# Optimization experiments

Measured on AMD Instinct MI355X. Metric: run time of the kernel, lower is better.

Reference implementation:

```python
import jax, jax.numpy as jnp
import numpy as np

N_HEAD = 16
N_EMBD = 2048
HEAD_DIM = N_EMBD // N_HEAD  # 128
B, T = 4, 2048
BASE_THETA = 10000.0


def _rotary_tables(seq_len, dim, dtype):
    inv_freq = 1.0 / (BASE_THETA ** (jnp.arange(0, dim, 2, dtype=jnp.float32) / dim))
    t = jnp.arange(seq_len, dtype=jnp.float32)
    freqs = jnp.outer(t, inv_freq)  # [T, dim/2]
    cos = jnp.cos(freqs)[None, :, None, :].astype(dtype)
    sin = jnp.sin(freqs)[None, :, None, :].astype(dtype)
    return cos, sin


def _apply_rotary(x, cos, sin):
    # x: [B, T, H, D]; rotate pairs (x[..., :D/2], x[..., D/2:])
    d = x.shape[3] // 2
    x1, x2 = x[..., :d], x[..., d:]
    y1 = x1 * cos + x2 * sin
    y2 = -x1 * sin + x2 * cos
    return jnp.concatenate([y1, y2], axis=3).astype(x.dtype)


def setup_inputs() -> dict:
    key = jax.random.key(0)
    ks = jax.random.split(key, 5)
    scale = 1.0 / np.sqrt(N_EMBD)
    return {
        "x": jax.random.normal(ks[0], (B, T, N_EMBD), dtype=jnp.float32),
        "wq": jax.random.normal(ks[1], (N_EMBD, N_EMBD), dtype=jnp.float32) * scale,
        "wk": jax.random.normal(ks[2], (N_EMBD, N_EMBD), dtype=jnp.float32) * scale,
        "wv": jax.random.normal(ks[3], (N_EMBD, N_EMBD), dtype=jnp.float32) * scale,
        "wo": jax.random.normal(ks[4], (N_EMBD, N_EMBD), dtype=jnp.float32) * scale,
    }


def reference(x, wq, wk, wv, wo):
    Bc, Tc, C = x.shape
    H, D = N_HEAD, HEAD_DIM
    # bias-free projections (nn.Linear applies x @ W.T)
    q = (x @ wq.T).reshape(Bc, Tc, H, D)
    k = (x @ wk.T).reshape(Bc, Tc, H, D)
    v = (x @ wv.T).reshape(Bc, Tc, H, D)
    cos, sin = _rotary_tables(Tc, D, x.dtype)
    # original module applies rotary TWICE (once before a dead SDPA, once after)
    q = _apply_rotary(_apply_rotary(q, cos, sin), cos, sin)
    k = _apply_rotary(_apply_rotary(k, cos, sin), cos, sin)
    # causal attention (flex_attention with causal block_mask, default scale)
    scores = jnp.einsum("bthd,bshd->bhts", q, k) / jnp.sqrt(jnp.asarray(D, x.dtype))
    causal = jnp.tril(jnp.ones((Tc, Tc), dtype=bool))
    scores = jnp.where(causal[None, None, :, :], scores, jnp.asarray(-jnp.inf, scores.dtype))
    attn = jax.nn.softmax(scores, axis=-1)
    y = jnp.einsum("bhts,bshd->bthd", attn, v).reshape(Bc, Tc, C)
    return y @ wo.T
```

## Files before the change

### kernel.cpp

```cpp
#include <hip/hip_runtime.h>
#include <math.h>

typedef unsigned short u16;
typedef __attribute__((ext_vector_type(4))) float f32x4;
typedef __attribute__((ext_vector_type(8))) __bf16 bf16x8;
typedef __attribute__((ext_vector_type(4))) unsigned short u16x4;
typedef __attribute__((ext_vector_type(8))) unsigned short u16x8;

#define GLL16(gp, lp) __builtin_amdgcn_global_load_lds( \
    (__attribute__((address_space(1))) void*)(void*)(gp), \
    (__attribute__((address_space(3))) void*)(void*)(lp), 16, 0, 0)

__device__ __forceinline__ u16 f2bf(float x) {
    unsigned u = __float_as_uint(x);
    return (u16)((u + 0x7FFFu + ((u >> 16) & 1u)) >> 16);
}
__device__ __forceinline__ float bf2f(u16 h) { return __uint_as_float(((unsigned)h) << 16); }

__device__ __forceinline__ f32x4 mfma16(bf16x8 a, bf16x8 b, f32x4 c) {
    return __builtin_amdgcn_mfma_f32_16x16x32_bf16(a, b, c, 0, 0, 0);
}

__global__ void cvt_f32_bf16(const float* __restrict__ s, u16* __restrict__ d, int n4) {
    int i = blockIdx.x * 256 + threadIdx.x;
    if (i < n4) {
        float4 v = ((const float4*)s)[i];
        u16x4 o = { f2bf(v.x), f2bf(v.y), f2bf(v.z), f2bf(v.w) };
        ((u16x4*)d)[i] = o;
    }
}

__global__ void rope_table_k(float2* __restrict__ tab) {
    int id = blockIdx.x * 256 + threadIdx.x;
    int t = id >> 6, j = id & 63;
    float freq = exp2f(-((float)(2 * j) / 128.f) * 13.287712379549449f);
    float ang = 2.f * (float)t * freq;
    float sv, cv;
    sincosf(ang, &sv, &cv);
    float2 r; r.x = cv; r.y = sv;
    tab[id] = r;
}

template <int MODE>
__global__ __launch_bounds__(256) void gemm_nt(const u16* __restrict__ A, const u16* __restrict__ Bw,
                                               u16* __restrict__ Qo, u16* __restrict__ Ko,
                                               u16* __restrict__ Vt, float* __restrict__ Out,
                                               const float2* __restrict__ tab, float qscale, int K) {
    __shared__ u16 smem[32768];
    const int tid = threadIdx.x;
    const int lane = tid & 63;
    const int qd = lane >> 4, ln = lane & 15;
    const int wid = tid >> 6;
    const int wx = wid & 1, wy = wid >> 1;

    constexpr int NBY = (MODE == 0) ? 48 : 16;
    const int id = blockIdx.y * 64 + blockIdx.x;
    const int xcd = id & 7, slot = id >> 3;
    const int m0 = ((slot / NBY) * 8 + xcd) * 128;
    const int n0 = (slot % NBY) * 128;

    int asrc[4], bsrc[4], ldst[4];
#pragma unroll
    for (int l = 0; l < 4; ++l) {
        const int i = l * 256 + tid;
        const int r = i >> 3;
        const int kc = (i & 7) ^ (r & 7);
        asrc[l] = (m0 + r) * K + kc * 8;
        bsrc[l] = (n0 + r) * K + kc * 8;
        ldst[l] = i * 8;
    }
    const u16* Ag = A;
    const u16* Bg = Bw;

    f32x4 acc[4][4];
#pragma unroll
    for (int mi = 0; mi < 4; ++mi)
#pragma unroll
        for (int ni = 0; ni < 4; ++ni) acc[mi][ni] = f32x4{0.f, 0.f, 0.f, 0.f};

    const int arow = (wy * 64 + ln) * 64;
    const int brow = (wx * 64 + ln) * 64;
    const int cx[2] = { (qd ^ (ln & 7)) * 8, ((qd + 4) ^ (ln & 7)) * 8 };

    auto compute = [&](int buf) {
        const u16* As = &smem[buf * 16384];
        const u16* Bs = As + 8192;
#pragma unroll
        for (int ks = 0; ks < 2; ++ks) {
            bf16x8 af[4], bfr[4];
#pragma unroll
            for (int i = 0; i < 4; ++i) af[i] = *(const bf16x8*)&As[arow + i * 1024 + cx[ks]];
#pragma unroll
            for (int i = 0; i < 4; ++i) bfr[i] = *(const bf16x8*)&Bs[brow + i * 1024 + cx[ks]];
#pragma unroll
            for (int mi = 0; mi < 4; ++mi)
#pragma unroll
                for (int ni = 0; ni < 4; ++ni)
                    acc[mi][ni] = mfma16(af[mi], bfr[ni], acc[mi][ni]);
        }
    };

    const int niter = K >> 6;
#pragma unroll
    for (int l = 0; l < 4; ++l) GLL16(Ag + asrc[l], &smem[ldst[l]]);
#pragma unroll
    for (int l = 0; l < 4; ++l) GLL16(Bg + bsrc[l], &smem[8192 + ldst[l]]);
    Ag += 64; Bg += 64;

    for (int kt = 0; kt < niter - 1; ++kt) {
        asm volatile("s_barrier" ::: "memory");
        u16* dA = &smem[((kt + 1) & 1) * 16384];
#pragma unroll
        for (int l = 0; l < 4; ++l) GLL16(Ag + asrc[l], &dA[ldst[l]]);
#pragma unroll
        for (int l = 0; l < 4; ++l) GLL16(Bg + bsrc[l], &dA[8192 + ldst[l]]);
        Ag += 64; Bg += 64;
        asm volatile("s_waitcnt vmcnt(8)" ::: "memory");
        asm volatile("s_barrier" ::: "memory");
        compute(kt & 1);
    }
    asm volatile("s_barrier" ::: "memory");
    asm volatile("s_waitcnt vmcnt(0)" ::: "memory");
    asm volatile("s_barrier" ::: "memory");
    compute((niter - 1) & 1);

    __syncthreads();

    if constexpr (MODE == 0) {
        const int sec = n0 >> 11;
        if (sec <= 1) {
#pragma unroll
            for (int mi = 0; mi < 4; ++mi)
#pragma unroll
                for (int ni = 0; ni < 4; ++ni) {
                    const int col = wx * 64 + ni * 16 + ln;
                    const int cc = col >> 3, co = col & 7;
#pragma unroll
                    for (int r = 0; r < 4; ++r) {
                        const int row = wy * 64 + mi * 16 + qd * 4 + r;
                        smem[row * 128 + ((cc ^ (row & 15)) * 8) + co] = f2bf(acc[mi][ni][r]);
                    }
                }
            __syncthreads();
            const float qs = (sec == 0) ? qscale : 1.0f;
            u16* dstb = (sec == 0 ? Qo : Ko);
#pragma unroll
            for (int it = 0; it < 4; ++it) {
                const int c = it * 256 + tid;
                const int m = c >> 3, d8 = c & 7;
                const u16x8 lo = *(const u16x8*)&smem[m * 128 + ((d8 ^ (m & 15)) * 8)];
                const u16x8 hi = *(const u16x8*)&smem[m * 128 + (((d8 + 8) ^ (m & 15)) * 8)];
                const int t = (m0 + m) & 2047;
                const float2* tb = tab + t * 64 + d8 * 8;
                u16x8 o1, o2;
#pragma unroll
                for (int i = 0; i < 8; ++i) {
                    const float x1 = bf2f(lo[i]), x2 = bf2f(hi[i]);
                    const float2 cs = tb[i];
                    o1[i] = f2bf((x1 * cs.x + x2 * cs.y) * qs);
                    o2[i] = f2bf((x2 * cs.x - x1 * cs.y) * qs);
                }
                u16* dst = dstb + (size_t)(m0 + m) * 2048 + (n0 & 2047) + d8 * 8;
                *(u16x8*)dst = o1;
                *(u16x8*)(dst + 64) = o2;
            }
        } else {
            const int bb = m0 >> 11;
#pragma unroll
            for (int mi = 0; mi < 4; ++mi) {
                const int mbase = wy * 64 + mi * 16 + qd * 4;
                const int mch = mbase >> 3, moff = mbase & 7;
#pragma unroll
                for (int ni = 0; ni < 4; ++ni) {
                    const int nl = wx * 64 + ni * 16 + ln;
                    u16x4 pk = { f2bf(acc[mi][ni][0]), f2bf(acc[mi][ni][1]),
                                 f2bf(acc[mi][ni][2]), f2bf(acc[mi][ni][3]) };
                    *(u16x4*)&smem[nl * 128 + ((mch ^ (nl & 15)) * 8) + moff] = pk;
                }
            }
            __syncthreads();
#pragma unroll
            for (int i = 0; i < 8; ++i) {
                const int c = i * 256 + tid;
                const int nl = c >> 4;
                const u16x8 v = *(const u16x8*)&smem[c * 8];
                const int mch = (c & 15) ^ (nl & 15);
                const int hd = (n0 - 4096) + nl;
                *(u16x8*)&Vt[((size_t)(bb * 2048 + hd)) * 2048 + (m0 & 2047) + mch * 8] = v;
            }
        }
    } else {
        const int mg0 = m0 + wy * 64 + qd * 4;
        const int ng0 = n0 + wx * 64 + ln;
#pragma unroll
        for (int mi = 0; mi < 4; ++mi)
#pragma unroll
            for (int ni = 0; ni < 4; ++ni) {
                const int ng = ng0 + ni * 16;
#pragma unroll
                for (int r = 0; r < 4; ++r)
                    Out[(size_t)(mg0 + mi * 16 + r) * 2048 + ng] = acc[mi][ni][r];
            }
    }
}

__global__ __launch_bounds__(512, 4) void attn_kernel(const u16* __restrict__ Qb, const u16* __restrict__ Kb,
                                                      const u16* __restrict__ Vt, u16* __restrict__ Yb) {
    extern __shared__ u16 smem[];
    u16* QP = smem;
    u16* KsB = smem + 8192;
    u16* VsB = smem + 8192 + 16384;

    const int tid = threadIdx.x;
    const int lane = tid & 63;
    const int qd = lane >> 4, ln = lane & 15;
    const int wid = tid >> 6;
    const int id = (int)blockIdx.x;
    const int px = id >> 6;
    const int bh = id & 63;
    const int b = bh >> 4, h = bh & 15;

    const u16* Qbh = Qb + ((size_t)b * 2048 * 16 + h) * 128;
    const u16* Kbh = Kb + ((size_t)b * 2048 * 16 + h) * 128;
    const u16* Vbh = Vt + ((size_t)(b * 16 + h) * 128) * 2048;

    int lC[2], kOff[2], vOff[2];
#pragma unroll
    for (int p = 0; p < 2; ++p) {
        const int c = p * 512 + tid;
        lC[p] = c * 8;
        { const int r = c >> 4, cc = (c & 15) ^ (r & 7); kOff[p] = r * 2048 + cc * 8; }
        { const int rv = c >> 3, cc = (c & 7) ^ (rv & 7); vOff[p] = rv * 2048 + cc * 8; }
    }

    bf16x8 onesf;
#pragma unroll
    for (int i = 0; i < 8; ++i) onesf[i] = (__bf16)1.0f;

    for (int half = 0; half < 2; ++half) {
        const int qt = half ? px : (15 - px);
        const int q0 = qt * 128;
        const int wq = q0 + wid * 16;
        const int nkt = 2 * qt + 2;

        __syncthreads();
#pragma unroll
        for (int p = 0; p < 2; ++p)
            GLL16(Qbh + (size_t)q0 * 2048 + kOff[p], &QP[lC[p]]);
        __syncthreads();
        bf16x8 qf[4];
        if (wid < 4) {
            const int lr = wid * 16 + ln;
#pragma unroll
            for (int ks = 0; ks < 4; ++ks)
                qf[ks] = *(const bf16x8*)&QP[lr * 128 + (((ks * 4 + qd) ^ (lr & 7)) * 8)];
        }
        __syncthreads();
#pragma unroll
        for (int p = 0; p < 2; ++p)
            GLL16(Qbh + (size_t)(q0 + 64) * 2048 + kOff[p], &QP[lC[p]]);
        __syncthreads();
        if (wid >= 4) {
            const int lr = (wid - 4) * 16 + ln;
#pragma unroll
            for (int ks = 0; ks < 4; ++ks)
                qf[ks] = *(const bf16x8*)&QP[lr * 128 + (((ks * 4 + qd) ^ (lr & 7)) * 8)];
        }
        __syncthreads();

#pragma unroll
        for (int p = 0; p < 2; ++p) GLL16(Kbh + kOff[p], &KsB[lC[p]]);
#pragma unroll
        for (int p = 0; p < 2; ++p) GLL16(Vbh + vOff[p], &VsB[lC[p]]);

        f32x4 o[8];
#pragma unroll
        for (int di = 0; di < 8; ++di) o[di] = f32x4{0.f, 0.f, 0.f, 0.f};
        f32x4 lacc = f32x4{0.f, 0.f, 0.f, 0.f};
        float Mr[4];
#pragma unroll
        for (int r = 0; r < 4; ++r) Mr[r] = -1e30f;

        for (int kt = 0; kt < nkt; ++kt) {
            const int k0 = kt * 64;
            asm volatile("s_barrier" ::: "memory");
            if (kt + 1 < nkt) {
                u16* kd = KsB + ((kt + 1) & 1) * 8192;
                u16* vd = VsB + ((kt + 1) & 1) * 8192;
#pragma unroll
                for (int p = 0; p < 2; ++p) GLL16(Kbh + (size_t)(k0 + 64) * 2048 + kOff[p], &kd[lC[p]]);
#pragma unroll
                for (int p = 0; p < 2; ++p) GLL16(Vbh + (size_t)(k0 + 64) + vOff[p], &vd[lC[p]]);
                asm volatile("s_waitcnt vmcnt(4)" ::: "memory");
            } else {
                asm volatile("s_waitcnt vmcnt(0)" ::: "memory");
            }
            asm volatile("s_barrier" ::: "memory");

            if (k0 <= wq + 15) {
                const u16* Kc = KsB + (kt & 1) * 8192;
                const u16* Vc = VsB + (kt & 1) * 8192;
                f32x4 s[4];
#pragma unroll
                for (int ni = 0; ni < 4; ++ni) s[ni] = f32x4{0.f, 0.f, 0.f, 0.f};
#pragma unroll
                for (int ks = 0; ks < 4; ++ks) {
                    bf16x8 kf[4];
#pragma unroll
                    for (int ni = 0; ni < 4; ++ni) {
                        const int row = ni * 16 + ln;
                        kf[ni] = *(const bf16x8*)&Kc[row * 128 + (((ks * 4 + qd) ^ (ln & 7)) * 8)];
                    }
#pragma unroll
                    for (int ni = 0; ni < 4; ++ni)
                        s[ni] = mfma16(qf[ks], kf[ni], s[ni]);
                }
                if (k0 + 63 > wq) {
#pragma unroll
                    for (int ni = 0; ni < 4; ++ni)
#pragma unroll
                        for (int r = 0; r < 4; ++r) {
                            const int qi = wq + qd * 4 + r;
                            const int ki = k0 + ni * 16 + ln;
                            if (ki > qi) s[ni][r] = -1e30f;
                        }
                }
                float rx[4];
#pragma unroll
                for (int r = 0; r < 4; ++r)
                    rx[r] = fmaxf(fmaxf(s[0][r], s[1][r]), fmaxf(s[2][r], s[3][r]));
#pragma unroll
                for (int st = 1; st < 16; st <<= 1)
#pragma unroll
                    for (int r = 0; r < 4; ++r)
                        rx[r] = fmaxf(rx[r], __shfl_xor(rx[r], st));
                float al[4];
                bool need = false;
#pragma unroll
                for (int r = 0; r < 4; ++r) {
                    const float nm = fmaxf(Mr[r], rx[r]);
                    al[r] = exp2f(Mr[r] - nm);
                    Mr[r] = nm;
                    need |= (al[r] != 1.0f);
                }
                if (__any(need)) {
#pragma unroll
                    for (int r = 0; r < 4; ++r) lacc[r] *= al[r];
#pragma unroll
                    for (int di = 0; di < 8; ++di)
#pragma unroll
                        for (int r = 0; r < 4; ++r) o[di][r] *= al[r];
                }
#pragma unroll
                for (int ni = 0; ni < 4; ++ni) {
                    const int cc0 = ni * 2 + (ln >> 3);
#pragma unroll
                    for (int r = 0; r < 4; ++r) {
                        const float p = exp2f(s[ni][r] - Mr[r]);
                        const int prow = wid * 16 + qd * 4 + r;
                        QP[prow * 64 + ((cc0 ^ ((prow >> 1) & 7)) * 8) + (ln & 7)] = f2bf(p);
                    }
                }
#pragma unroll
                for (int ks2 = 0; ks2 < 2; ++ks2) {
                    const int prow = wid * 16 + ln;
                    bf16x8 pf = *(const bf16x8*)&QP[prow * 64 + (((ks2 * 4 + qd) ^ ((prow >> 1) & 7)) * 8)];
                    lacc = mfma16(pf, onesf, lacc);
#pragma unroll
                    for (int di = 0; di < 8; ++di) {
                        const int row = di * 16 + ln;
                        bf16x8 vf = *(const bf16x8*)&Vc[row * 64 + (((ks2 * 4 + qd) ^ (ln & 7)) * 8)];
                        o[di] = mfma16(pf, vf, o[di]);
                    }
                }
            }
        }

        float inv[4];
#pragma unroll
        for (int r = 0; r < 4; ++r) inv[r] = 1.f / lacc[r];
#pragma unroll
        for (int di = 0; di < 8; ++di)
#pragma unroll
            for (int r = 0; r < 4; ++r) {
                const int t = q0 + wid * 16 + qd * 4 + r;
                const int d = di * 16 + ln;
                Yb[((size_t)((b * 2048 + t) * 16 + h)) * 128 + d] = f2bf(o[di][r] * inv[r]);
            }
    }
}

extern "C" void kernel_launch(void* const* d_in, const int* in_sizes, int n_in,
                              void* d_out, int out_size, void* d_ws, size_t ws_size,
                              hipStream_t stream) {
    const float* x  = (const float*)d_in[0];
    const float* wq = (const float*)d_in[1];
    const float* wk = (const float*)d_in[2];
    const float* wv = (const float*)d_in[3];
    const float* wo = (const float*)d_in[4];
    float* out = (float*)d_out;
    char* ws = (char*)d_ws;

    u16* xb     = (u16*)(ws);
    u16* wqkv   = (u16*)(ws + (size_t)33554432);
    u16* wob    = (u16*)(ws + (size_t)58720256);
    u16* Qb     = (u16*)(ws + (size_t)67108864);
    u16* Kb     = (u16*)(ws + (size_t)100663296);
    u16* Vt     = (u16*)(ws + (size_t)134217728);
    float2* tab = (float2*)(ws + (size_t)167772160);
    u16* Yb = xb;

    const float scl = 0.08838834764831845f * 1.4426950408889634f;

    cvt_f32_bf16<<<16384, 256, 0, stream>>>(x, xb, 4194304);
    cvt_f32_bf16<<<4096, 256, 0, stream>>>(wq, wqkv, 1048576);
    cvt_f32_bf16<<<4096, 256, 0, stream>>>(wk, wqkv + 4194304, 1048576);
    cvt_f32_bf16<<<4096, 256, 0, stream>>>(wv, wqkv + 8388608, 1048576);
    cvt_f32_bf16<<<4096, 256, 0, stream>>>(wo, wob, 1048576);
    rope_table_k<<<512, 256, 0, stream>>>(tab);

    gemm_nt<0><<<dim3(64, 48), 256, 0, stream>>>(xb, wqkv, Qb, Kb, Vt, nullptr, tab, scl, 2048);

    hipFuncSetAttribute((const void*)attn_kernel, hipFuncAttributeMaxDynamicSharedMemorySize, 81920);
    attn_kernel<<<dim3(512), 512, 81920, stream>>>(Qb, Kb, Vt, Yb);

    gemm_nt<1><<<dim3(64, 16), 256, 0, stream>>>(Yb, wob, nullptr, nullptr, nullptr, out, tab, 1.0f, 2048);
}
```

Measured before the change: 641.3 us.

## Enlarge GEMM tiles to 256x256 with 8 waves and quarter-staged prefetch pipeline

Both projection GEMMs now use 256x256 output tiles computed by 512-thread blocks, each wave owning a 128x64 sub-tile, with 128KB of dynamic LDS for double buffering. The K loop is split into four MFMA phases. Each phase issues the prefetch of one quarter of the next tile and raises wave priority around the MFMA bursts. The aim is more data reuse per LDS load and better overlap of global loads with compute. In exchange, the grid has fewer blocks (768 and 256), so the output GEMM may not fill all CUs, and register pressure is higher.

```diff
diff --git a/kernel.cpp b/kernel.cpp
--- a/kernel.cpp
+++ b/kernel.cpp
@@ -42,114 +42,157 @@
 }
 
 template <int MODE>
-__global__ __launch_bounds__(256) void gemm_nt(const u16* __restrict__ A, const u16* __restrict__ Bw,
-                                               u16* __restrict__ Qo, u16* __restrict__ Ko,
-                                               u16* __restrict__ Vt, float* __restrict__ Out,
-                                               const float2* __restrict__ tab, float qscale, int K) {
-    __shared__ u16 smem[32768];
+__global__ __launch_bounds__(512, 2) void gemm_nt(const u16* __restrict__ A, const u16* __restrict__ Bw,
+                                                  u16* __restrict__ Qo, u16* __restrict__ Ko,
+                                                  u16* __restrict__ Vt, float* __restrict__ Out,
+                                                  const float2* __restrict__ tab, float qscale, int K) {
+    extern __shared__ u16 smem[];
     const int tid = threadIdx.x;
     const int lane = tid & 63;
     const int qd = lane >> 4, ln = lane & 15;
     const int wid = tid >> 6;
-    const int wx = wid & 1, wy = wid >> 1;
-
-    constexpr int NBY = (MODE == 0) ? 48 : 16;
-    const int id = blockIdx.y * 64 + blockIdx.x;
+    const int wr = wid >> 2, wc = wid & 3;
+
+    constexpr int NBY = (MODE == 0) ? 24 : 8;
+    const int id = (int)blockIdx.x;
     const int xcd = id & 7, slot = id >> 3;
-    const int m0 = ((slot / NBY) * 8 + xcd) * 128;
-    const int n0 = (slot % NBY) * 128;
-
-    int asrc[4], bsrc[4], ldst[4];
-#pragma unroll
-    for (int l = 0; l < 4; ++l) {
-        const int i = l * 256 + tid;
-        const int r = i >> 3;
-        const int kc = (i & 7) ^ (r & 7);
-        asrc[l] = (m0 + r) * K + kc * 8;
-        bsrc[l] = (n0 + r) * K + kc * 8;
-        ldst[l] = i * 8;
-    }
-    const u16* Ag = A;
-    const u16* Bg = Bw;
-
-    f32x4 acc[4][4];
-#pragma unroll
-    for (int mi = 0; mi < 4; ++mi)
+    const int m0 = ((slot / NBY) * 8 + xcd) * 256;
+    const int n0 = (slot % NBY) * 256;
+
+    int sr[2], skc[2];
+#pragma unroll
+    for (int l = 0; l < 2; ++l) {
+        const int i = l * 512 + tid;
+        sr[l] = i >> 3;
+        skc[l] = (i & 7) ^ (sr[l] & 7);
+    }
+
+    auto stage = [&](int tt, int hx) {
+        const u16* gp = (hx < 2) ? A : Bw;
+        const int x0 = (hx < 2) ? m0 : n0;
+        const int h = hx & 1;
+        u16* lb = &smem[(tt & 1) * 32768 + (hx >> 1) * 16384 + h * 8192];
+#pragma unroll
+        for (int l = 0; l < 2; ++l)
+            GLL16(gp + (size_t)(x0 + 128 * h + sr[l]) * K + tt * 64 + skc[l] * 8,
+                  &lb[(l * 512 + tid) * 8]);
+    };
+
+    f32x4 acc[8][4];
+#pragma unroll
+    for (int mi = 0; mi < 8; ++mi)
 #pragma unroll
         for (int ni = 0; ni < 4; ++ni) acc[mi][ni] = f32x4{0.f, 0.f, 0.f, 0.f};
 
-    const int arow = (wy * 64 + ln) * 64;
-    const int brow = (wx * 64 + ln) * 64;
-    const int cx[2] = { (qd ^ (ln & 7)) * 8, ((qd + 4) ^ (ln & 7)) * 8 };
-
-    auto compute = [&](int buf) {
-        const u16* As = &smem[buf * 16384];
-        const u16* Bs = As + 8192;
-#pragma unroll
-        for (int ks = 0; ks < 2; ++ks) {
-            bf16x8 af[4], bfr[4];
-#pragma unroll
-            for (int i = 0; i < 4; ++i) af[i] = *(const bf16x8*)&As[arow + i * 1024 + cx[ks]];
-#pragma unroll
-            for (int i = 0; i < 4; ++i) bfr[i] = *(const bf16x8*)&Bs[brow + i * 1024 + cx[ks]];
-#pragma unroll
-            for (int mi = 0; mi < 4; ++mi)
-#pragma unroll
-                for (int ni = 0; ni < 4; ++ni)
-                    acc[mi][ni] = mfma16(af[mi], bfr[ni], acc[mi][ni]);
-        }
-    };
+    const int arow = (wr * 128 + ln) * 64;
+    const int brow = (wc * 64 + ln) * 64;
+    const int cxk[2] = { (qd ^ (ln & 7)) * 8, ((qd + 4) ^ (ln & 7)) * 8 };
 
     const int niter = K >> 6;
-#pragma unroll
-    for (int l = 0; l < 4; ++l) GLL16(Ag + asrc[l], &smem[ldst[l]]);
-#pragma unroll
-    for (int l = 0; l < 4; ++l) GLL16(Bg + bsrc[l], &smem[8192 + ldst[l]]);
-    Ag += 64; Bg += 64;
-
-    for (int kt = 0; kt < niter - 1; ++kt) {
+    stage(0, 0); stage(0, 1); stage(0, 2); stage(0, 3);
+    stage(1, 0);
+
+#pragma unroll 2
+    for (int t = 0; t < niter; ++t) {
+        const u16* As = &smem[(t & 1) * 32768];
+        const u16* Bs = As + 16384;
+        const bool pf = (t + 1 < niter);
+        if (pf) asm volatile("s_waitcnt vmcnt(2)" ::: "memory");
+        else    asm volatile("s_waitcnt vmcnt(0)" ::: "memory");
         asm volatile("s_barrier" ::: "memory");
-        u16* dA = &smem[((kt + 1) & 1) * 16384];
-#pragma unroll
-        for (int l = 0; l < 4; ++l) GLL16(Ag + asrc[l], &dA[ldst[l]]);
-#pragma unroll
-        for (int l = 0; l < 4; ++l) GLL16(Bg + bsrc[l], &dA[8192 + ldst[l]]);
-        Ag += 64; Bg += 64;
-        asm volatile("s_waitcnt vmcnt(8)" ::: "memory");
+        bf16x8 a0[4][2], b0[2][2];
+#pragma unroll
+        for (int mi = 0; mi < 4; ++mi)
+#pragma unroll
+            for (int ks = 0; ks < 2; ++ks)
+                a0[mi][ks] = *(const bf16x8*)&As[arow + mi * 1024 + cxk[ks]];
+#pragma unroll
+        for (int ni = 0; ni < 2; ++ni)
+#pragma unroll
+            for (int ks = 0; ks < 2; ++ks)
+                b0[ni][ks] = *(const bf16x8*)&Bs[brow + ni * 1024 + cxk[ks]];
+        if (pf) stage(t + 1, 1);
+        __builtin_amdgcn_s_setprio(1);
+#pragma unroll
+        for (int mi = 0; mi < 4; ++mi)
+#pragma unroll
+            for (int ni = 0; ni < 2; ++ni)
+#pragma unroll
+                for (int ks = 0; ks < 2; ++ks)
+                    acc[mi][ni] = mfma16(a0[mi][ks], b0[ni][ks], acc[mi][ni]);
+        __builtin_amdgcn_s_setprio(0);
         asm volatile("s_barrier" ::: "memory");
-        compute(kt & 1);
-    }
-    asm volatile("s_barrier" ::: "memory");
-    asm volatile("s_waitcnt vmcnt(0)" ::: "memory");
-    asm volatile("s_barrier" ::: "memory");
-    compute((niter - 1) & 1);
-
+        bf16x8 b1[2][2];
+#pragma unroll
+        for (int ni = 0; ni < 2; ++ni)
+#pragma unroll
+            for (int ks = 0; ks < 2; ++ks)
+                b1[ni][ks] = *(const bf16x8*)&Bs[brow + (ni + 2) * 1024 + cxk[ks]];
+        if (pf) stage(t + 1, 2);
+        __builtin_amdgcn_s_setprio(1);
+#pragma unroll
+        for (int mi = 0; mi < 4; ++mi)
+#pragma unroll
+            for (int ni = 0; ni < 2; ++ni)
+#pragma unroll
+                for (int ks = 0; ks < 2; ++ks)
+                    acc[mi][ni + 2] = mfma16(a0[mi][ks], b1[ni][ks], acc[mi][ni + 2]);
+        __builtin_amdgcn_s_setprio(0);
+        asm volatile("s_barrier" ::: "memory");
+        bf16x8 a1[4][2];
+#pragma unroll
+        for (int mi = 0; mi < 4; ++mi)
+#pragma unroll
+            for (int ks = 0; ks < 2; ++ks)
+                a1[mi][ks] = *(const bf16x8*)&As[arow + (mi + 4) * 1024 + cxk[ks]];
+        if (pf) stage(t + 1, 3);
+        __builtin_amdgcn_s_setprio(1);
+#pragma unroll
+        for (int mi = 0; mi < 4; ++mi)
+#pragma unroll
+            for (int ni = 0; ni < 2; ++ni)
+#pragma unroll
+                for (int ks = 0; ks < 2; ++ks)
+                    acc[mi + 4][ni] = mfma16(a1[mi][ks], b0[ni][ks], acc[mi + 4][ni]);
+        __builtin_amdgcn_s_setprio(0);
+        asm volatile("s_barrier" ::: "memory");
+        if (t + 2 < niter) stage(t + 2, 0);
+        __builtin_amdgcn_s_setprio(1);
+#pragma unroll
+        for (int mi = 0; mi < 4; ++mi)
+#pragma unroll
+            for (int ni = 0; ni < 2; ++ni)
+#pragma unroll
+                for (int ks = 0; ks < 2; ++ks)
+                    acc[mi + 4][ni + 2] = mfma16(a1[mi][ks], b1[ni][ks], acc[mi + 4][ni + 2]);
+        __builtin_amdgcn_s_setprio(0);
+    }
     __syncthreads();
 
     if constexpr (MODE == 0) {
         const int sec = n0 >> 11;
         if (sec <= 1) {
 #pragma unroll
-            for (int mi = 0; mi < 4; ++mi)
+            for (int mi = 0; mi < 8; ++mi)
 #pragma unroll
                 for (int ni = 0; ni < 4; ++ni) {
-                    const int col = wx * 64 + ni * 16 + ln;
+                    const int col = wc * 64 + ni * 16 + ln;
                     const int cc = col >> 3, co = col & 7;
 #pragma unroll
                     for (int r = 0; r < 4; ++r) {
-                        const int row = wy * 64 + mi * 16 + qd * 4 + r;
-                        smem[row * 128 + ((cc ^ (row & 15)) * 8) + co] = f2bf(acc[mi][ni][r]);
+                        const int row = wr * 128 + mi * 16 + qd * 4 + r;
+                        smem[row * 256 + ((cc ^ (row & 15)) * 8) + co] = f2bf(acc[mi][ni][r]);
                     }
                 }
             __syncthreads();
             const float qs = (sec == 0) ? qscale : 1.0f;
             u16* dstb = (sec == 0 ? Qo : Ko);
 #pragma unroll
-            for (int it = 0; it < 4; ++it) {
-                const int c = it * 256 + tid;
-                const int m = c >> 3, d8 = c & 7;
-                const u16x8 lo = *(const u16x8*)&smem[m * 128 + ((d8 ^ (m & 15)) * 8)];
-                const u16x8 hi = *(const u16x8*)&smem[m * 128 + (((d8 + 8) ^ (m & 15)) * 8)];
+            for (int it = 0; it < 8; ++it) {
+                const int c = it * 512 + tid;
+                const int m = c >> 4, hh = (c >> 3) & 1, d8 = c & 7;
+                const u16x8 lo = *(const u16x8*)&smem[m * 256 + (((hh * 16 + d8) ^ (m & 15)) * 8)];
+                const u16x8 hi = *(const u16x8*)&smem[m * 256 + (((hh * 16 + 8 + d8) ^ (m & 15)) * 8)];
                 const int t = (m0 + m) & 2047;
                 const float2* tb = tab + t * 64 + d8 * 8;
                 u16x8 o1, o2;
@@ -160,40 +203,40 @@
                     o1[i] = f2bf((x1 * cs.x + x2 * cs.y) * qs);
                     o2[i] = f2bf((x2 * cs.x - x1 * cs.y) * qs);
                 }
-                u16* dst = dstb + (size_t)(m0 + m) * 2048 + (n0 & 2047) + d8 * 8;
+                u16* dst = dstb + (size_t)(m0 + m) * 2048 + (n0 & 2047) + hh * 128 + d8 * 8;
                 *(u16x8*)dst = o1;
                 *(u16x8*)(dst + 64) = o2;
             }
         } else {
             const int bb = m0 >> 11;
 #pragma unroll
-            for (int mi = 0; mi < 4; ++mi) {
-                const int mbase = wy * 64 + mi * 16 + qd * 4;
+            for (int mi = 0; mi < 8; ++mi) {
+                const int mbase = wr * 128 + mi * 16 + qd * 4;
                 const int mch = mbase >> 3, moff = mbase & 7;
 #pragma unroll
                 for (int ni = 0; ni < 4; ++ni) {
-                    const int nl = wx * 64 + ni * 16 + ln;
+                    const int nl = wc * 64 + ni * 16 + ln;
                     u16x4 pk = { f2bf(acc[mi][ni][0]), f2bf(acc[mi][ni][1]),
                                  f2bf(acc[mi][ni][2]), f2bf(acc[mi][ni][3]) };
-                    *(u16x4*)&smem[nl * 128 + ((mch ^ (nl & 15)) * 8) + moff] = pk;
+                    *(u16x4*)&smem[nl * 256 + ((mch ^ (nl & 15)) * 8) + moff] = pk;
                 }
             }
             __syncthreads();
 #pragma unroll
-            for (int i = 0; i < 8; ++i) {
-                const int c = i * 256 + tid;
-                const int nl = c >> 4;
-                const u16x8 v = *(const u16x8*)&smem[c * 8];
-                const int mch = (c & 15) ^ (nl & 15);
+            for (int i = 0; i < 16; ++i) {
+                const int c = i * 512 + tid;
+                const int nl = c >> 5, ch = c & 31;
+                const u16x8 v = *(const u16x8*)&smem[nl * 256 + ch * 8];
+                const int mch = ch ^ (nl & 15);
                 const int hd = (n0 - 4096) + nl;
                 *(u16x8*)&Vt[((size_t)(bb * 2048 + hd)) * 2048 + (m0 & 2047) + mch * 8] = v;
             }
         }
     } else {
-        const int mg0 = m0 + wy * 64 + qd * 4;
-        const int ng0 = n0 + wx * 64 + ln;
-#pragma unroll
-        for (int mi = 0; mi < 4; ++mi)
+        const int mg0 = m0 + wr * 128 + qd * 4;
+        const int ng0 = n0 + wc * 64 + ln;
+#pragma unroll
+        for (int mi = 0; mi < 8; ++mi)
 #pragma unroll
             for (int ni = 0; ni < 4; ++ni) {
                 const int ng = ng0 + ni * 16;
@@ -419,10 +462,13 @@
     cvt_f32_bf16<<<4096, 256, 0, stream>>>(wo, wob, 1048576);
     rope_table_k<<<512, 256, 0, stream>>>(tab);
 
-    gemm_nt<0><<<dim3(64, 48), 256, 0, stream>>>(xb, wqkv, Qb, Kb, Vt, nullptr, tab, scl, 2048);
+    hipFuncSetAttribute((const void*)gemm_nt<0>, hipFuncAttributeMaxDynamicSharedMemorySize, 131072);
+    hipFuncSetAttribute((const void*)gemm_nt<1>, hipFuncAttributeMaxDynamicSharedMemorySize, 131072);
+
+    gemm_nt<0><<<dim3(768), 512, 131072, stream>>>(xb, wqkv, Qb, Kb, Vt, nullptr, tab, scl, 2048);
 
     hipFuncSetAttribute((const void*)attn_kernel, hipFuncAttributeMaxDynamicSharedMemorySize, 81920);
     attn_kernel<<<dim3(512), 512, 81920, stream>>>(Qb, Kb, Vt, Yb);
 
-    gemm_nt<1><<<dim3(64, 16), 256, 0, stream>>>(Yb, wob, nullptr, nullptr, nullptr, out, tab, 1.0f, 2048);
-}
+    gemm_nt<1><<<dim3(256), 512, 131072, stream>>>(Yb, wob, nullptr, nullptr, nullptr, out, tab, 1.0f, 2048);
+}
```

New measurement: 546.0 us. -14.9%, faster.
